# Optimization experiments

Measured on AMD Instinct MI355X. Metric: run time of the kernel, lower is better.

Reference implementation:

```python
import jax, jax.numpy as jnp
import numpy as np
from jax import lax

S = 2048      # services
MAXL = 16     # max exec steps per service
D = 4096      # devices
RN = 128      # size_realnode
HN = 128      # size_hypernode
HEADS = 4
CH = RN + HN  # 256
NRO = 256     # readout neurons
NITER = 3
NEG = 0.2     # leaky relu slope


def _gru(x, h, Wih, Whh, bih, bhh):
    # PyTorch GRU/GRUCell equations, gate order (r, z, n)
    gi = x @ Wih + bih
    gh = h @ Whh + bhh
    ir, iz, ig = jnp.split(gi, 3, axis=-1)
    hr, hz, hg = jnp.split(gh, 3, axis=-1)
    r = jax.nn.sigmoid(ir + hr)
    z = jax.nn.sigmoid(iz + hz)
    n = jnp.tanh(ig + r * hg)
    return (1.0 - z) * n + z * h


def _mlp(x, W1, b1, W2, b2, W3, b3):
    # Linear-ReLU-(Dropout eval=id)-Linear-ReLU-Linear
    h = jax.nn.relu(x @ W1 + b1)
    h = jax.nn.relu(h @ W2 + b2)
    return h @ W3 + b3


def forward(realnode, arr, exeSeqs, index_devices, index_fragments, frag2dev_node, frag2dev_row, lengths, frag_service, frag_pos,
            W_dev, b_dev, W_frg, b_frg, W_srv, b_srv,
            C_Wih, C_Whh, C_bih, C_bhh, F_Wih, F_Whh, F_bih, F_bhh, D_Wih, D_Whh, D_bih, D_bhh,
            W_src, b_src, W_tgt, b_tgt, att, bias_att,
            Wt1, bt1, Wt2, bt2, Wt3, bt3, Wl1, bl1, Wl2, bl2, Wl3, bl3):
    nodes = realnode.shape[0] + 1          # row 0 is zero-pad row (1-based node ids)
    Sn, L2 = exeSeqs.shape
    L = L2 // 2
    Dn = index_devices.shape[0]
    dtype = realnode.dtype

    # initial real-node states (scatter with disjoint indices == set)
    devs = realnode[index_devices - 1] @ W_dev + b_dev
    frags = realnode[index_fragments - 1] @ W_frg + b_frg
    state = jnp.zeros((nodes, RN), dtype).at[index_devices].set(devs).at[index_fragments].set(frags)

    h_srv = arr @ W_srv + b_srv            # [S, HN] GRU hidden (torch shape [1,S,HN])
    frag_state = state[index_fragments]

    for _ in range(NITER):
        # phiC: packed GRU over per-service execution sequences
        seq = state[exeSeqs].reshape(Sn, L, 2 * RN)   # [S, L, 2*RN]

        def step(h, xt_t):
            xt, t = xt_t
            hn = _gru(xt, h, C_Wih, C_Whh, C_bih, C_bhh)
            h = jnp.where((t < lengths)[:, None], hn, h)  # packed semantics: freeze past length
            return h, h

        h_srv, outs = lax.scan(step, h_srv, (seq.transpose(1, 0, 2), jnp.arange(L)))
        outs = outs.transpose(1, 0, 2)                # [S, L, HN]
        out_f = outs[frag_service, frag_pos]          # [F, HN] valid steps only (extract_indices)

        # messageF: hypernode output || state of device hosting the fragment
        msgF = jnp.concatenate([out_f, state[frag2dev_node]], axis=-1)   # [F, HN+RN]
        frag_state = state[index_fragments]
        frag_old = frag_state
        frag_state = _gru(msgF, frag_state, F_Wih, F_Whh, F_bih, F_bhh)

        # GAT-style scatter softmax over devices
        src = (jnp.concatenate([out_f, frag_old], axis=-1) @ W_src + b_src).reshape(-1, HEADS, CH)  # [F,H,CH]
        dev_state = state[index_devices]
        tgt = (dev_state @ W_tgt + b_tgt).reshape(-1, HEADS, CH)                                    # [D,H,CH]
        e = jax.nn.leaky_relu(src + tgt[frag2dev_row], NEG)
        alpha = (e * att).sum(-1)                                        # [F, HEADS]
        amax = jax.ops.segment_max(alpha, frag2dev_row, num_segments=Dn)
        w = jnp.exp(alpha - amax[frag2dev_row])
        wsum = jax.ops.segment_sum(w, frag2dev_row, num_segments=Dn)
        a = w / (wsum[frag2dev_row] + 1e-16)
        msgD = jax.ops.segment_sum(src * a[:, :, None], frag2dev_row, num_segments=Dn)
        msgD = msgD.mean(axis=1) + bias_att                              # [D, CH]
        dev_state = _gru(msgD, dev_state, D_Wih, D_Whh, D_bih, D_bhh)

        state = jnp.zeros((nodes, RN), dtype).at[index_devices].set(dev_state).at[index_fragments].set(frag_state)

    # mean-pool fragment states per service
    pooled = jax.ops.segment_sum(frag_state, frag_service, num_segments=Sn) / lengths[:, None].astype(dtype)
    latency = _mlp(pooled, Wl1, bl1, Wl2, bl2, Wl3, bl3)[:, 0]           # [S]
    thr = _mlp(h_srv, Wt1, bt1, Wt2, bt2, Wt3, bt3)[:, 0]                # [S]
    return jnp.concatenate([latency, thr])[None, :]                      # [1, 2S]


def setup_inputs() -> dict:
    lengths_np = np.tile(np.array([4, 8, 12, 16], dtype=np.int64), S // 4)
    F = int(lengths_np.sum())            # 20480 fragments
    num_real = D + F                     # 24576
    rng = np.random.RandomState(0)
    frag2dev_row = rng.randint(0, D, size=F).astype(np.int64)       # device row per fragment
    frag_service = np.repeat(np.arange(S, dtype=np.int64), lengths_np)
    frag_pos = np.concatenate([np.arange(l, dtype=np.int64) for l in lengths_np])
    index_devices = np.arange(1, D + 1, dtype=np.int64)             # 1-based node ids
    index_fragments = np.arange(D + 1, D + F + 1, dtype=np.int64)
    dev_node = frag2dev_row + 1
    exeSeqs = np.zeros((S, 2 * MAXL), dtype=np.int64)               # pad with 0 (zero row)
    exeSeqs[frag_service, 2 * frag_pos] = index_fragments
    exeSeqs[frag_service, 2 * frag_pos + 1] = dev_node

    keys = iter(jax.random.split(jax.random.key(0), 64))
    def rn(shape, s=0.05):
        return jax.random.normal(next(keys), shape, jnp.float32) * s
    z = lambda *sh: jnp.zeros(sh, jnp.float32)

    return {
        'realnode': rn((num_real, 5), 1.0), 'arr': rn((S, 5), 1.0),
        'exeSeqs': jnp.asarray(exeSeqs), 'index_devices': jnp.asarray(index_devices),
        'index_fragments': jnp.asarray(index_fragments), 'frag2dev_node': jnp.asarray(dev_node),
        'frag2dev_row': jnp.asarray(frag2dev_row), 'lengths': jnp.asarray(lengths_np),
        'frag_service': jnp.asarray(frag_service), 'frag_pos': jnp.asarray(frag_pos),
        'W_dev': rn((5, RN), 0.3), 'b_dev': z(RN), 'W_frg': rn((5, RN), 0.3), 'b_frg': z(RN),
        'W_srv': rn((5, HN), 0.3), 'b_srv': z(HN),
        'C_Wih': rn((2 * RN, 3 * HN)), 'C_Whh': rn((HN, 3 * HN)), 'C_bih': z(3 * HN), 'C_bhh': z(3 * HN),
        'F_Wih': rn((CH, 3 * RN)), 'F_Whh': rn((RN, 3 * RN)), 'F_bih': z(3 * RN), 'F_bhh': z(3 * RN),
        'D_Wih': rn((CH, 3 * RN)), 'D_Whh': rn((RN, 3 * RN)), 'D_bih': z(3 * RN), 'D_bhh': z(3 * RN),
        'W_src': rn((CH, HEADS * CH)), 'b_src': z(HEADS * CH),
        'W_tgt': rn((RN, HEADS * CH)), 'b_tgt': z(HEADS * CH),
        'att': rn((1, HEADS, CH), 0.1), 'bias_att': z(CH),
        'Wt1': rn((HN, NRO)), 'bt1': z(NRO), 'Wt2': rn((NRO, NRO)), 'bt2': z(NRO), 'Wt3': rn((NRO, 1)), 'bt3': z(1),
        'Wl1': rn((RN, NRO)), 'bl1': z(NRO), 'Wl2': rn((NRO, NRO)), 'bl2': z(NRO), 'Wl3': rn((NRO, 1)), 'bl3': z(1),
    }


def reference(realnode, arr, exeSeqs, index_devices, index_fragments, frag2dev_node, frag2dev_row, lengths, frag_service, frag_pos,
              W_dev, b_dev, W_frg, b_frg, W_srv, b_srv,
              C_Wih, C_Whh, C_bih, C_bhh, F_Wih, F_Whh, F_bih, F_bhh, D_Wih, D_Whh, D_bih, D_bhh,
              W_src, b_src, W_tgt, b_tgt, att, bias_att,
              Wt1, bt1, Wt2, bt2, Wt3, bt3, Wl1, bl1, Wl2, bl2, Wl3, bl3):
    return forward(realnode, arr, exeSeqs, index_devices, index_fragments, frag2dev_node, frag2dev_row, lengths, frag_service, frag_pos,
                   W_dev, b_dev, W_frg, b_frg, W_srv, b_srv,
                   C_Wih, C_Whh, C_bih, C_bhh, F_Wih, F_Whh, F_bih, F_bhh, D_Wih, D_Whh, D_bih, D_bhh,
                   W_src, b_src, W_tgt, b_tgt, att, bias_att,
                   Wt1, bt1, Wt2, bt2, Wt3, bt3, Wl1, bl1, Wl2, bl2, Wl3, bl3)
```

## Files before the change

kernel.cpp:

```cpp
#include <hip/hip_runtime.h>
#include <hip/hip_bf16.h>

typedef __attribute__((ext_vector_type(8))) short bf16x8;
typedef __attribute__((ext_vector_type(4))) float f32x4;

__device__ __forceinline__ float sigf(float x){ return 1.0f/(1.0f+expf(-x)); }
__device__ __forceinline__ int clampi(int v, int lo, int hi){ return v<lo?lo:(v>hi?hi:v); }
__device__ __forceinline__ unsigned short f2b(float f){
    __hip_bfloat16 h = __float2bfloat16(f);
    return *reinterpret_cast<unsigned short*>(&h);
}
__device__ __forceinline__ float us2f(unsigned short u){ return __uint_as_float(((unsigned)u)<<16); }

__device__ __forceinline__ void gload16(const void* g, void* l){
    __builtin_amdgcn_global_load_lds((const __attribute__((address_space(1))) void*)g,
                                     (__attribute__((address_space(3))) void*)l, 16, 0, 0);
}

__global__ void k_cvt(const int* __restrict__ src, int* __restrict__ dst, int n,
                      const int* __restrict__ det)
{
    int i = blockIdx.x*blockDim.x + threadIdx.x;
    if (i >= n) return;
    int stride = (det[1] == 0) ? 2 : 1;
    dst[i] = src[(size_t)i*stride];
}

__global__ void k_wt(const float* __restrict__ W, unsigned short* __restrict__ Wt,
                     int N, int kshift, int kmask, int total)
{
    int idx = blockIdx.x*blockDim.x + threadIdx.x;
    if (idx >= total) return;
    int n = idx >> kshift, k = idx & kmask;
    Wt[idx] = f2b(W[(size_t)k*N + n]);
}

__global__ void k_wt2(const float* __restrict__ W, unsigned short* __restrict__ Whi,
                      unsigned short* __restrict__ Wlo, int N, int kshift, int kmask, int total)
{
    int idx = blockIdx.x*blockDim.x + threadIdx.x;
    if (idx >= total) return;
    int n = idx >> kshift, k = idx & kmask;
    float v = W[(size_t)k*N + n];
    unsigned short hi = f2b(v);
    Whi[idx] = hi;
    Wlo[idx] = f2b(v - us2f(hi));
}

__global__ void k_proj5(const float* __restrict__ X, const float* __restrict__ W,
                        const float* __restrict__ bias,
                        const int* __restrict__ gidx, const int* __restrict__ sidx,
                        float* __restrict__ out, unsigned short* __restrict__ outBf,
                        float* __restrict__ out2, unsigned short* __restrict__ out2Bf,
                        int M, int nrows, int nodes)
{
    int t = blockIdx.x*blockDim.x + threadIdx.x;
    int i = t >> 7, j = t & 127;
    if (i >= M) return;
    int src = gidx ? clampi(gidx[i]-1, 0, nrows-1) : i;
    const float* xp = X + (size_t)src*5;
    float acc = bias[j];
#pragma unroll
    for (int k=0;k<5;k++) acc += xp[k] * W[k*128+j];
    int dr = sidx ? clampi(sidx[i], 0, nodes-1) : i;
    if (out)   out[(size_t)dr*128 + j] = acc;
    if (outBf) outBf[(size_t)dr*128 + j] = f2b(acc);
    if (out2)  out2[(size_t)i*128 + j] = acc;
    if (out2Bf) out2Bf[(size_t)i*128 + j] = f2b(acc);
}

__launch_bounds__(256)
__global__ void k_mm(const float* __restrict__ A0, int lda,
                     const float* __restrict__ B, int ldb,
                     const float* __restrict__ bias, float* __restrict__ C,
                     int M, int N, int K, int relu, float scale, int accum)
{
    __shared__ float As[16][132];
    __shared__ float Bs[16][132];
    int tid = threadIdx.x;
    int tx = tid & 15, ty = tid >> 4;
    int row0 = blockIdx.y * 128, col0 = blockIdx.x * 128;
    float acc[8][8] = {};
    for (int k0 = 0; k0 < K; k0 += 16){
#pragma unroll
        for (int q = 0; q < 2; ++q){
            int idx = tid + q*256;
            int r = idx >> 2, k4 = (idx & 3) * 4;
            const float* src = A0 + (size_t)(row0+r)*lda + k0 + k4;
            float4 v = *reinterpret_cast<const float4*>(src);
            As[k4+0][r]=v.x; As[k4+1][r]=v.y; As[k4+2][r]=v.z; As[k4+3][r]=v.w;
        }
#pragma unroll
        for (int q = 0; q < 2; ++q){
            int idx = tid + q*256;
            int kb = idx >> 5, n4 = (idx & 31) * 4;
            float4 v = *reinterpret_cast<const float4*>(B + (size_t)(k0+kb)*ldb + col0 + n4);
            *reinterpret_cast<float4*>(&Bs[kb][n4]) = v;
        }
        __syncthreads();
#pragma unroll
        for (int k = 0; k < 16; ++k){
            float a[8], b[8];
            *(float4*)&a[0] = *(const float4*)&As[k][ty*8];
            *(float4*)&a[4] = *(const float4*)&As[k][ty*8+4];
            *(float4*)&b[0] = *(const float4*)&Bs[k][tx*8];
            *(float4*)&b[4] = *(const float4*)&Bs[k][tx*8+4];
#pragma unroll
            for (int i=0;i<8;i++)
#pragma unroll
                for (int j=0;j<8;j++) acc[i][j] += a[i]*b[j];
        }
        __syncthreads();
    }
    float bb[8];
#pragma unroll
    for (int j=0;j<8;j++) bb[j] = bias ? bias[col0+tx*8+j] : 0.f;
#pragma unroll
    for (int i=0;i<8;i++){
        float* cp = C + (size_t)(row0+ty*8+i)*N + col0 + tx*8;
#pragma unroll
        for (int jq=0;jq<2;jq++){
            float4 prev = accum ? *(const float4*)(cp+jq*4) : make_float4(0,0,0,0);
            float o[4];
#pragma unroll
            for (int c=0;c<4;c++){
                float u = acc[i][jq*4+c] + bb[jq*4+c];
                if (relu) u = fmaxf(u,0.f);
                o[c] = (&prev.x)[c] + scale*u;
            }
            *(float4*)(cp+jq*4) = make_float4(o[0],o[1],o[2],o[3]);
        }
    }
}

struct MJob {
    const unsigned short *A0, *A1;
    const int *i0, *i1;
    const unsigned short *Wt;
    const float *bias;
    void *C;
    int N, K, epi, nrow;
    float scale;
};

#define MM2_SMEM 67840

__device__ __forceinline__ void mm2_body(const MJob J, int bid, char* smem)
{
    unsigned short* AsB = (unsigned short*)smem;
    unsigned short* BsB = AsB + 16384;
    int tid = threadIdx.x;
    int l = tid & 63, w = tid >> 6;
    int wr = w >> 1, wc = w & 1;
    int row0 = (bid % J.nrow) * 128, col0 = (bid / J.nrow) * 128;
    int nK = J.K >> 6;

    f32x4 acc[4][4];
#pragma unroll
    for (int m=0;m<4;m++)
#pragma unroll
        for (int n=0;n<4;n++) acc[m][n] = (f32x4){0.f,0.f,0.f,0.f};

    auto stage = [&](int buf, int k0){
        unsigned short* As = AsB + buf*8192;
        unsigned short* Bs = BsB + buf*8192;
#pragma unroll
        for (int q=0;q<4;q++){
            int slot = q*256 + w*64 + l;
            int r = slot >> 3, c8 = slot & 7;
            int g8 = c8 ^ (r & 7);
            int row; const unsigned short* base; int kl;
            if (k0 < 128){ row = J.i0 ? J.i0[row0+r] : (row0+r); base = J.A0; kl = k0; }
            else         { row = J.i1 ? J.i1[row0+r] : (row0+r); base = J.A1; kl = k0-128; }
            const char* g = (const char*)(base + (size_t)row*128 + kl) + g8*16;
            gload16(g, (void*)&As[(size_t)(q*256 + w*64)*8]);
        }
#pragma unroll
        for (int q=0;q<4;q++){
            int slot = q*256 + w*64 + l;
            int n = slot >> 3, kc = slot & 7;
            int g8 = kc ^ (n & 7);
            const char* g = (const char*)(J.Wt + (size_t)(col0+n)*J.K + k0) + g8*16;
            gload16(g, (void*)&Bs[(size_t)(q*256 + w*64)*8]);
        }
    };

    stage(0, 0);
    for (int ks=0; ks<nK; ++ks){
        int cur = ks & 1;
        if (ks+1 < nK){
            stage(cur^1, (ks+1)*64);
            asm volatile("s_waitcnt vmcnt(8)" ::: "memory");
        } else {
            asm volatile("s_waitcnt vmcnt(0)" ::: "memory");
        }
        __builtin_amdgcn_s_barrier();
        __builtin_amdgcn_sched_barrier(0);
        unsigned short* As = AsB + cur*8192;
        unsigned short* Bs = BsB + cur*8192;
#pragma unroll
        for (int kk = 0; kk < 2; ++kk){
            int ek = kk*32 + (l >> 4) * 8;
            bf16x8 af[4], bf[4];
#pragma unroll
            for (int m=0;m<4;m++){
                int r = wr*64 + m*16 + (l & 15);
                af[m] = *reinterpret_cast<const bf16x8*>(&As[r*64 + (ek ^ ((r & 7) << 3))]);
            }
#pragma unroll
            for (int n=0;n<4;n++){
                int c = wc*64 + n*16 + (l & 15);
                bf[n] = *reinterpret_cast<const bf16x8*>(&Bs[c*64 + (ek ^ ((c & 7) << 3))]);
            }
#pragma unroll
            for (int m=0;m<4;m++)
#pragma unroll
                for (int n=0;n<4;n++)
                    acc[m][n] = __builtin_amdgcn_mfma_f32_16x16x32_bf16(af[m], bf[n], acc[m][n], 0, 0, 0);
        }
        __builtin_amdgcn_sched_barrier(0);
        __builtin_amdgcn_s_barrier();
    }

    if (J.epi == 0){
        float* Ct = (float*)smem;
#pragma unroll
        for (int m=0;m<4;m++){
#pragma unroll
            for (int v=0;v<4;v++){
                int rl = wr*64 + m*16 + (l >> 4)*4 + v;
#pragma unroll
                for (int n=0;n<4;n++){
                    int c = wc*64 + n*16 + (l & 15);
                    Ct[rl*132 + c] = J.scale*acc[m][n][v] + (J.bias ? J.bias[col0+c] : 0.f);
                }
            }
        }
        __syncthreads();
#pragma unroll
        for (int q=0;q<16;q++){
            int idx = tid + q*256;
            int r = idx >> 5, c4 = (idx & 31)*4;
            float4 v = *reinterpret_cast<const float4*>(&Ct[r*132 + c4]);
            *reinterpret_cast<float4*>((float*)J.C + (size_t)(row0+r)*J.N + col0 + c4) = v;
        }
    } else {
        unsigned short* Cb = (unsigned short*)smem;
#pragma unroll
        for (int m=0;m<4;m++){
#pragma unroll
            for (int v=0;v<4;v++){
                int rl = wr*64 + m*16 + (l >> 4)*4 + v;
#pragma unroll
                for (int n=0;n<4;n++){
                    int c = wc*64 + n*16 + (l & 15);
                    Cb[rl*136 + c] = f2b(J.scale*acc[m][n][v] + (J.bias ? J.bias[col0+c] : 0.f));
                }
            }
        }
        __syncthreads();
#pragma unroll
        for (int q=0;q<8;q++){
            int idx = tid + q*256;
            int r = idx >> 4, c8 = (idx & 15)*8;
            uint4 v = *reinterpret_cast<const uint4*>(&Cb[r*136 + c8]);
            *reinterpret_cast<uint4*>((unsigned short*)J.C + (size_t)(row0+r)*J.N + col0 + c8) = v;
        }
    }
}

__launch_bounds__(256)
__global__ void mm2one(MJob a)
{
    __shared__ alignas(16) char smem[MM2_SMEM];
    mm2_body(a, blockIdx.x, smem);
}

__launch_bounds__(256)
__global__ void mm2two(MJob a, MJob b, int asplit)
{
    __shared__ alignas(16) char smem[MM2_SMEM];
    int bid = blockIdx.x;
    if (bid < asplit) mm2_body(a, bid, smem);
    else              mm2_body(b, bid - asplit, smem);
}

struct GJob {
    const unsigned short *A0, *A1;
    const int *i0, *i1;
    int lda;
    const unsigned short *Wih, *Whh;
    const float *bih, *bhh;
    float *H;
    unsigned short *Hbf, *stateBf;
    const int *sidx;
    int M, nodes;
};

__device__ __forceinline__ void gru_body(const GJob J, int bid, char* smem)
{
    unsigned short* AsB = (unsigned short*)smem;
    unsigned short* BsB = AsB + 2*8192;
    int tid = threadIdx.x;
    int l = tid & 63, w = tid >> 6;
    int row0 = bid * 128;
    f32x4 acc[24], accN[8];
#pragma unroll
    for (int n=0;n<24;n++) acc[n] = (f32x4){0.f,0.f,0.f,0.f};
#pragma unroll
    for (int n=0;n<8;n++) accN[n] = (f32x4){0.f,0.f,0.f,0.f};

    auto stage = [&](int buf, int st){
        int k0 = st*64;
        unsigned short* As = AsB + buf*8192;
        unsigned short* Bs = BsB + buf*24576;
#pragma unroll
        for (int q=0;q<2;q++){
            int slot = q*512 + w*64 + l;
            int r = slot >> 3, c8 = slot & 7;
            int g8 = c8 ^ (r & 7);
            const unsigned short* src;
            if (st < 4){
                if (J.i1){
                    if (k0 < 128){ int ri = J.i0 ? J.i0[row0+r] : (row0+r); src = J.A0 + (size_t)ri*128 + k0; }
                    else         { int ri = J.i1[row0+r]; src = J.A1 + (size_t)ri*128 + (k0-128); }
                } else {
                    src = J.A0 + (size_t)(row0+r)*J.lda + k0;
                }
            } else {
                src = J.Hbf + (size_t)(row0+r)*128 + (k0-256);
            }
            gload16((const char*)src + g8*16, (void*)&As[(size_t)(q*512 + w*64)*8]);
        }
#pragma unroll
        for (int q=0;q<6;q++){
            int slot = q*512 + w*64 + l;
            int n = slot >> 3, kc = slot & 7;
            int g8 = kc ^ (n & 7);
            const unsigned short* src = (st < 4) ? (J.Wih + (size_t)n*256 + k0)
                                                 : (J.Whh + (size_t)n*128 + (k0-256));
            gload16((const char*)src + g8*16, (void*)&Bs[(size_t)(q*512 + w*64)*8]);
        }
    };

    stage(0, 0);
    for (int st=0; st<6; ++st){
        int cur = st & 1;
        if (st+1 < 6){
            stage(cur^1, st+1);
            asm volatile("s_waitcnt vmcnt(8)" ::: "memory");
        } else {
            asm volatile("s_waitcnt vmcnt(0)" ::: "memory");
        }
        __builtin_amdgcn_s_barrier();
        __builtin_amdgcn_sched_barrier(0);
        unsigned short* As = AsB + cur*8192;
        unsigned short* Bs = BsB + cur*24576;
        if (st < 4){
#pragma unroll
            for (int kk=0; kk<2; ++kk){
                int ek = kk*32 + (l >> 4)*8;
                int r = w*16 + (l & 15);
                bf16x8 af = *reinterpret_cast<const bf16x8*>(&As[r*64 + (ek ^ ((r & 7) << 3))]);
#pragma unroll
                for (int n=0;n<24;n++){
                    int c = n*16 + (l & 15);
                    bf16x8 bf = *reinterpret_cast<const bf16x8*>(&Bs[c*64 + (ek ^ ((c & 7) << 3))]);
                    acc[n] = __builtin_amdgcn_mfma_f32_16x16x32_bf16(af, bf, acc[n], 0, 0, 0);
                }
            }
        } else {
#pragma unroll
            for (int kk=0; kk<2; ++kk){
                int ek = kk*32 + (l >> 4)*8;
                int r = w*16 + (l & 15);
                bf16x8 af = *reinterpret_cast<const bf16x8*>(&As[r*64 + (ek ^ ((r & 7) << 3))]);
#pragma unroll
                for (int n=0;n<24;n++){
                    int c = n*16 + (l & 15);
                    bf16x8 bf = *reinterpret_cast<const bf16x8*>(&Bs[c*64 + (ek ^ ((c & 7) << 3))]);
                    if (n < 16) acc[n]     = __builtin_amdgcn_mfma_f32_16x16x32_bf16(af, bf, acc[n], 0, 0, 0);
                    else        accN[n-16] = __builtin_amdgcn_mfma_f32_16x16x32_bf16(af, bf, accN[n-16], 0, 0, 0);
                }
            }
        }
        __builtin_amdgcn_sched_barrier(0);
        __builtin_amdgcn_s_barrier();
    }

    __syncthreads();
    float* Hld = (float*)smem;
    unsigned short* Hb = (unsigned short*)(smem + 67584);
#pragma unroll
    for (int q=0;q<8;q++){
        int idx = tid + q*512;
        int r = idx >> 5, c4 = (idx & 31)*4;
        float4 v = *reinterpret_cast<const float4*>(J.H + (size_t)(row0+r)*128 + c4);
        *reinterpret_cast<float4*>(&Hld[r*132 + c4]) = v;
    }
    __syncthreads();
#pragma unroll
    for (int v=0;v<4;v++){
        int rl = w*16 + (l >> 4)*4 + v;
#pragma unroll
        for (int c=0;c<8;c++){
            int col = c*16 + (l & 15);
            float rr = sigf(acc[c][v]    + J.bih[col]     + J.bhh[col]);
            float zz = sigf(acc[c+8][v]  + J.bih[col+128] + J.bhh[col+128]);
            float nn = tanhf(acc[c+16][v] + J.bih[col+256] + rr*(accN[c][v] + J.bhh[col+256]));
            float hv = Hld[rl*132 + col];
            float hn = (1.f-zz)*nn + zz*hv;
            Hld[rl*132 + col] = hn;
            Hb[rl*136 + col] = f2b(hn);
        }
    }
    __syncthreads();
#pragma unroll
    for (int q=0;q<8;q++){
        int idx = tid + q*512;
        int r = idx >> 5, c4 = (idx & 31)*4;
        float4 v = *reinterpret_cast<const float4*>(&Hld[r*132 + c4]);
        *reinterpret_cast<float4*>(J.H + (size_t)(row0+r)*128 + c4) = v;
    }
#pragma unroll
    for (int q=0;q<4;q++){
        int idx = tid + q*512;
        int r = idx >> 4, c8 = (idx & 15)*8;
        uint4 v = *reinterpret_cast<const uint4*>(&Hb[r*136 + c8]);
        *reinterpret_cast<uint4*>(J.Hbf + (size_t)(row0+r)*128 + c8) = v;
        int st = clampi(J.sidx[row0+r],0,J.nodes-1);
        *reinterpret_cast<uint4*>(J.stateBf + (size_t)st*128 + c8) = v;
    }
}

__launch_bounds__(512)
__global__ void gru2(GJob a, GJob b, int asplit)
{
    __shared__ alignas(16) char smem[131072];
    int bid = blockIdx.x;
    if (bid < asplit) gru_body(a, bid, smem);
    else              gru_body(b, bid - asplit, smem);
}

__launch_bounds__(256)
__global__ void k_attn(const unsigned short* __restrict__ SRC, const unsigned short* __restrict__ tgtbf,
                       const float* __restrict__ att, const int* __restrict__ list,
                       const int* __restrict__ offs, const float* __restrict__ batt,
                       unsigned short* __restrict__ msgDbf,
                       float* __restrict__ alphaG, int Dn, int F)
{
    __shared__ float tg[1024];
    __shared__ float alds[128*4];
    __shared__ float accs[4][256];
    int d = blockIdx.x;
    int tid = threadIdx.x;
    int w = tid >> 6, lane = tid & 63;
    for (int u = tid; u < 1024; u += 256) tg[u] = us2f(tgtbf[(size_t)d*1024 + u]);
    __syncthreads();
    int beg = offs[d], end = offs[d+1];
    if (beg < 0) beg = 0; if (end > F) end = F; if (end < beg) end = beg;
    int c0 = w*256 + lane*4;
    float t0 = tg[c0], t1 = tg[c0+1], t2 = tg[c0+2], t3 = tg[c0+3];
    float a0 = att[c0], a1 = att[c0+1], a2 = att[c0+2], a3 = att[c0+3];
    float amax = -3.4e38f;
    for (int i=beg;i<end;i++){
        int f = list[i];
        ushort4 sv = *reinterpret_cast<const ushort4*>(SRC + (size_t)f*1024 + c0);
        float e0 = us2f(sv.x)+t0, e1 = us2f(sv.y)+t1, e2 = us2f(sv.z)+t2, e3 = us2f(sv.w)+t3;
        e0 = e0>0.f?e0:0.2f*e0; e1 = e1>0.f?e1:0.2f*e1;
        e2 = e2>0.f?e2:0.2f*e2; e3 = e3>0.f?e3:0.2f*e3;
        float s = e0*a0 + e1*a1 + e2*a2 + e3*a3;
#pragma unroll
        for (int msk=1; msk<64; msk<<=1) s += __shfl_xor(s, msk);
        int li = i - beg;
        if (li < 128){ if (lane == 0) alds[li*4+w] = s; }
        else         { if (lane == 0) alphaG[(size_t)f*4+w] = s; }
        amax = fmaxf(amax, s);
    }
    __syncthreads();
    float wsum = 0.f;
    for (int i=beg;i<end;i++){
        int li = i - beg;
        float a = (li < 128) ? alds[li*4+w] : alphaG[(size_t)list[i]*4+w];
        wsum += expf(a - amax);
    }
    float iws = 1.f/(wsum + 1e-16f);
    float acc[4] = {0,0,0,0};
    for (int i=beg;i<end;i++){
        int f = list[i];
        int li = i - beg;
        float a = (li < 128) ? alds[li*4+w] : alphaG[(size_t)f*4+w];
        float p = expf(a - amax)*iws;
        ushort4 sv = *reinterpret_cast<const ushort4*>(SRC + (size_t)f*1024 + c0);
        acc[0] += p*us2f(sv.x); acc[1] += p*us2f(sv.y);
        acc[2] += p*us2f(sv.z); acc[3] += p*us2f(sv.w);
    }
#pragma unroll
    for (int j=0;j<4;j++) accs[w][lane*4+j] = acc[j];
    __syncthreads();
    if (tid < 256){
        float m = (accs[0][tid]+accs[1][tid]+accs[2][tid]+accs[3][tid])*0.25f + batt[tid];
        msgDbf[(size_t)d*256 + tid] = f2b(m);
    }
}

__launch_bounds__(512)
__global__ void k_recur(float* __restrict__ h_srv, const unsigned short* __restrict__ giFb,
                        const unsigned short* __restrict__ Whi,
                        const unsigned short* __restrict__ Wlo,
                        const float* __restrict__ bhh,
                        const int* __restrict__ inv,
                        unsigned short* __restrict__ out_f_bf,
                        int S, int L, int F)
{
    __shared__ float hs[8][129];
    __shared__ alignas(16) unsigned short hsHi[16*128];
    __shared__ alignas(16) unsigned short hsLo[16*128];
    __shared__ float ghs[16][385];
    __shared__ int fLoc[16][8];
    int tid = threadIdx.x;
    int l = tid & 63, w = tid >> 6;
    int lane15 = l & 15, lhi = l >> 4;
    int s0 = blockIdx.x * 8;
    for (int u = tid; u < 2048; u += 512){
        int s=u>>7,k=u&127;
        int ksw = k ^ ((s & 7) << 3);
        if (s < 8){
            float v = h_srv[(size_t)(s0+s)*128+k];
            hs[s][k] = v;
            unsigned short hb = f2b(v);
            hsHi[s*128 + ksw] = hb;
            hsLo[s*128 + ksw] = f2b(v - us2f(hb));
        } else {
            hsHi[s*128 + ksw] = 0;
            hsLo[s*128 + ksw] = 0;
        }
    }
    if (tid < 128) fLoc[tid>>3][tid&7] = inv[(size_t)(s0+(tid&7))*L + (tid>>3)];
    bf16x8 wHi[3][4], wLo[3][4];
#pragma unroll
    for (int ct=0; ct<3; ++ct){
        int col = w*48 + ct*16 + lane15;
#pragma unroll
        for (int ks=0; ks<4; ++ks){
            size_t off = (size_t)col*128 + ks*32 + lhi*8;
            wHi[ct][ks] = *reinterpret_cast<const bf16x8*>(Whi + off);
            wLo[ct][ks] = *reinterpret_cast<const bf16x8*>(Wlo + off);
        }
    }
    __syncthreads();
    for (int t=0;t<L;++t){
        bf16x8 hHi[4], hLo[4];
#pragma unroll
        for (int ks=0; ks<4; ++ks){
            int ek = ks*32 + lhi*8;
            int off = lane15*128 + (ek ^ ((lane15 & 7) << 3));
            hHi[ks] = *reinterpret_cast<const bf16x8*>(&hsHi[off]);
            hLo[ks] = *reinterpret_cast<const bf16x8*>(&hsLo[off]);
        }
#pragma unroll
        for (int ct=0; ct<3; ++ct){
            f32x4 acc = (f32x4){0.f,0.f,0.f,0.f};
#pragma unroll
            for (int ks=0; ks<4; ++ks){
                acc = __builtin_amdgcn_mfma_f32_16x16x32_bf16(hHi[ks], wHi[ct][ks], acc, 0,0,0);
                acc = __builtin_amdgcn_mfma_f32_16x16x32_bf16(hLo[ks], wHi[ct][ks], acc, 0,0,0);
                acc = __builtin_amdgcn_mfma_f32_16x16x32_bf16(hHi[ks], wLo[ct][ks], acc, 0,0,0);
            }
            int col = w*48 + ct*16 + lane15;
            float bb = bhh[col];
#pragma unroll
            for (int v=0; v<4; ++v){
                ghs[lhi*4 + v][col] = acc[v] + bb;
            }
        }
        __syncthreads();
        for (int u = tid; u < 1024; u += 512){
            int s=u>>7, k=u&127; int f = fLoc[t][s];
            if (f >= 0 && f < F){
                const unsigned short* gp = giFb + (size_t)f*384;
                float r  = sigf(us2f(gp[k])     + ghs[s][k]);
                float zz = sigf(us2f(gp[128+k]) + ghs[s][128+k]);
                float n  = tanhf(us2f(gp[256+k]) + r*ghs[s][256+k]);
                float hn = (1.f-zz)*n + zz*hs[s][k];
                hs[s][k] = hn;
                unsigned short hb = f2b(hn);
                int ksw = k ^ ((s & 7) << 3);
                hsHi[s*128 + ksw] = hb;
                hsLo[s*128 + ksw] = f2b(hn - us2f(hb));
                out_f_bf[(size_t)f*128+k] = hb;
            }
        }
        __syncthreads();
    }
    for (int u = tid; u < 1024; u += 512){ int s=u>>7,k=u&127; h_srv[(size_t)(s0+s)*128+k] = hs[s][k]; }
}

__global__ void k_count(const int* __restrict__ row, int* __restrict__ counts, int F, int Dn)
{ int f = blockIdx.x*blockDim.x + threadIdx.x; if (f < F) atomicAdd(&counts[clampi(row[f],0,Dn-1)], 1); }

__global__ void k_scan(const int* __restrict__ counts, int* __restrict__ offs, int D)
{
    __shared__ int part[257];
    int tid = threadIdx.x;
    int per = (D + 255) / 256;
    int s = 0;
    for (int i=0;i<per;i++){ int idx = tid*per+i; if (idx < D) s += counts[idx]; }
    part[tid] = s;
    __syncthreads();
    if (tid == 0){
        int acc = 0;
        for (int i=0;i<256;i++){ int v = part[i]; part[i] = acc; acc += v; }
        part[256] = acc;
    }
    __syncthreads();
    int acc = part[tid];
    for (int i=0;i<per;i++){ int idx = tid*per+i; if (idx < D){ offs[idx] = acc; acc += counts[idx]; } }
    if (tid == 0) offs[D] = part[256];
}

__global__ void k_fill(const int* __restrict__ row, const int* __restrict__ offs,
                       int* __restrict__ cursor, int* __restrict__ list, int F, int Dn)
{
    int f = blockIdx.x*blockDim.x + threadIdx.x;
    if (f >= F) return;
    int r = clampi(row[f],0,Dn-1);
    int p = atomicAdd(&cursor[r], 1);
    int pos = offs[r]+p;
    if (pos >= 0 && pos < F) list[pos] = f;
}

__global__ void k_build_inv(const int* __restrict__ fs, const int* __restrict__ fp,
                            int* __restrict__ inv, int F, int L, int S)
{
    int f = blockIdx.x*blockDim.x + threadIdx.x;
    if (f >= F) return;
    inv[clampi(fs[f],0,S-1)*L + clampi(fp[f],0,L-1)] = f;
}

__global__ void k_pool_add(const float* __restrict__ frag, const int* __restrict__ fs,
                           float* __restrict__ pooled, int F, int S)
{
    int t = blockIdx.x*blockDim.x + threadIdx.x;
    int i = t >> 7, j = t & 127;
    if (i >= F) return;
    atomicAdd(&pooled[(size_t)clampi(fs[i],0,S-1)*128 + j], frag[(size_t)i*128 + j]);
}

__global__ void k_pool_div(float* __restrict__ pooled, const int* __restrict__ lengths, int S)
{
    int t = blockIdx.x*blockDim.x + threadIdx.x;
    int i = t >> 7, j = t & 127;
    if (i >= S) return;
    int l = lengths[i]; if (l < 1) l = 1;
    pooled[(size_t)i*128 + j] /= (float)l;
}

__global__ void k_dot_out(const float* __restrict__ H, const float* __restrict__ W3,
                          const float* __restrict__ b3, float* __restrict__ outv, int off)
{
    __shared__ float red[256];
    int s = blockIdx.x, tid = threadIdx.x;
    red[tid] = H[(size_t)s*256 + tid] * W3[tid];
    __syncthreads();
    for (int st=128; st; st>>=1){ if (tid < st) red[tid] += red[tid+st]; __syncthreads(); }
    if (tid == 0) outv[off + s] = red[0] + b3[0];
}

extern "C" void kernel_launch(void* const* d_in, const int* in_sizes, int n_in,
                              void* d_out, int out_size, void* d_ws, size_t ws_size,
                              hipStream_t stream)
{
    (void)n_in; (void)out_size; (void)ws_size;
    const float* realnode = (const float*)d_in[0];
    const float* arr      = (const float*)d_in[1];
    const int* r_exe   = (const int*)d_in[2];
    const int* r_idev  = (const int*)d_in[3];
    const int* r_ifrag = (const int*)d_in[4];
    const int* r_fdn   = (const int*)d_in[5];
    const int* r_fdr   = (const int*)d_in[6];
    const int* r_len   = (const int*)d_in[7];
    const int* r_fsvc  = (const int*)d_in[8];
    const int* r_fpos  = (const int*)d_in[9];
    const float *W_dev=(const float*)d_in[10], *b_dev=(const float*)d_in[11];
    const float *W_frg=(const float*)d_in[12], *b_frg=(const float*)d_in[13];
    const float *W_srv=(const float*)d_in[14], *b_srv=(const float*)d_in[15];
    const float *C_Wih=(const float*)d_in[16], *C_Whh=(const float*)d_in[17], *C_bih=(const float*)d_in[18], *C_bhh=(const float*)d_in[19];
    const float *F_Wih=(const float*)d_in[20], *F_Whh=(const float*)d_in[21], *F_bih=(const float*)d_in[22], *F_bhh=(const float*)d_in[23];
    const float *D_Wih=(const float*)d_in[24], *D_Whh=(const float*)d_in[25], *D_bih=(const float*)d_in[26], *D_bhh=(const float*)d_in[27];
    const float *W_src=(const float*)d_in[28], *b_src=(const float*)d_in[29];
    const float *W_tgt=(const float*)d_in[30], *b_tgt=(const float*)d_in[31];
    const float *att=(const float*)d_in[32], *bias_att=(const float*)d_in[33];
    const float *Wt1=(const float*)d_in[34], *bt1=(const float*)d_in[35], *Wt2=(const float*)d_in[36], *bt2=(const float*)d_in[37], *Wt3=(const float*)d_in[38], *bt3=(const float*)d_in[39];
    const float *Wl1=(const float*)d_in[40], *bl1=(const float*)d_in[41], *Wl2=(const float*)d_in[42], *bl2=(const float*)d_in[43], *Wl3=(const float*)d_in[44], *bl3=(const float*)d_in[45];
    float* outp = (float*)d_out;

    const int S  = in_sizes[7];
    const int Dn = in_sizes[3];
    const int F  = in_sizes[4];
    const int L  = in_sizes[2] / (2*S);
    const int nreal = in_sizes[0]/5;
    const int nodes = nreal + 1;
    const int NIT = 3;

    char* wp = (char*)d_ws;
    auto alloc = [&](size_t nelem)->float*{
        float* p = (float*)wp;
        wp += ((nelem*4 + 255)/256)*256;
        return p;
    };
    float* h_srv  = alloc((size_t)S*128);
    float* fragA  = alloc((size_t)F*128);
    float* devA   = alloc((size_t)Dn*128);
    float* alphaB = alloc((size_t)F*4);
    float* UNION  = alloc((size_t)F*512);
    unsigned short* giFb = (unsigned short*)UNION;
    unsigned short* SRC  = (unsigned short*)UNION;
    float* Z      = alloc((size_t)Dn*1024);
    float* TGTf   = alloc((size_t)Dn*512);
    unsigned short* TGT = (unsigned short*)TGTf;
    float* pooled = alloc((size_t)S*128);
    unsigned short* state_bf = (unsigned short*)alloc((size_t)nodes*64);
    unsigned short* out_f_bf = (unsigned short*)alloc((size_t)F*64);
    unsigned short* fragA_bf = (unsigned short*)alloc((size_t)F*64);
    unsigned short* devA_bf  = (unsigned short*)alloc((size_t)Dn*64);
    unsigned short* msgD_bf  = (unsigned short*)alloc((size_t)Dn*128);
    unsigned short* tCWih   = (unsigned short*)alloc(384*256/2);
    unsigned short* tCWhhHi = (unsigned short*)alloc(384*128/2);
    unsigned short* tCWhhLo = (unsigned short*)alloc(384*128/2);
    unsigned short* tFWih   = (unsigned short*)alloc(384*256/2);
    unsigned short* tFWhh   = (unsigned short*)alloc(384*128/2);
    unsigned short* tDWih   = (unsigned short*)alloc(384*256/2);
    unsigned short* tDWhh   = (unsigned short*)alloc(384*128/2);
    unsigned short* tWtgt   = (unsigned short*)alloc(1024*128/2);
    unsigned short* tWsrc   = (unsigned short*)alloc(1024*256/2);
    int* cExe   = (int*)alloc((size_t)S*2*L);
    int* cIdev  = (int*)alloc((size_t)Dn);
    int* cIfrag = (int*)alloc((size_t)F);
    int* cFdn   = (int*)alloc((size_t)F);
    int* cFdr   = (int*)alloc((size_t)F);
    int* cLen   = (int*)alloc((size_t)S);
    int* cFsvc  = (int*)alloc((size_t)F);
    int* cFpos  = (int*)alloc((size_t)F);
    int* inv    = (int*)alloc((size_t)S*L);
    int* counts = (int*)alloc((size_t)Dn);
    int* offs   = (int*)alloc((size_t)Dn+1);
    int* cursor = (int*)alloc((size_t)Dn);
    int* list   = (int*)alloc((size_t)F);

    const int* det = r_idev;
    auto cvt = [&](const int* src, int* dst, int n){
        k_cvt<<<dim3((n+255)/256),256,0,stream>>>(src, dst, n, det);
    };
    cvt(r_exe,  cExe,  S*2*L);
    cvt(r_idev, cIdev, Dn);
    cvt(r_ifrag,cIfrag,F);
    cvt(r_fdn,  cFdn,  F);
    cvt(r_fdr,  cFdr,  F);
    cvt(r_len,  cLen,  S);
    cvt(r_fsvc, cFsvc, F);
    cvt(r_fpos, cFpos, F);

    k_wt<<<dim3((98304+255)/256),256,0,stream>>>(C_Wih, tCWih, 384, 8, 255, 98304);
    k_wt2<<<dim3((49152+255)/256),256,0,stream>>>(C_Whh, tCWhhHi, tCWhhLo, 384, 7, 127, 49152);
    k_wt<<<dim3((98304+255)/256),256,0,stream>>>(F_Wih, tFWih, 384, 8, 255, 98304);
    k_wt<<<dim3((49152+255)/256),256,0,stream>>>(F_Whh, tFWhh, 384, 7, 127, 49152);
    k_wt<<<dim3((98304+255)/256),256,0,stream>>>(D_Wih, tDWih, 384, 8, 255, 98304);
    k_wt<<<dim3((49152+255)/256),256,0,stream>>>(D_Whh, tDWhh, 384, 7, 127, 49152);
    k_wt<<<dim3((131072+255)/256),256,0,stream>>>(W_tgt, tWtgt, 1024, 7, 127, 131072);
    k_wt<<<dim3((262144+255)/256),256,0,stream>>>(W_src, tWsrc, 1024, 8, 255, 262144);

    hipMemsetAsync(state_bf, 0, (size_t)nodes*128*2, stream);
    hipMemsetAsync(inv, 0xFF, (size_t)S*L*4, stream);
    hipMemsetAsync(counts, 0, (size_t)Dn*4, stream);
    hipMemsetAsync(cursor, 0, (size_t)Dn*4, stream);

    k_proj5<<<dim3((Dn*128+255)/256),256,0,stream>>>(realnode, W_dev, b_dev, cIdev, cIdev,
        nullptr, state_bf, devA, devA_bf, Dn, nreal, nodes);
    k_proj5<<<dim3(((size_t)F*128+255)/256),256,0,stream>>>(realnode, W_frg, b_frg, cIfrag, cIfrag,
        nullptr, state_bf, fragA, fragA_bf, F, nreal, nodes);
    k_proj5<<<dim3((S*128+255)/256),256,0,stream>>>(arr, W_srv, b_srv, nullptr, nullptr,
        h_srv, nullptr, nullptr, nullptr, S, S, nodes);
    k_build_inv<<<dim3((F+255)/256),256,0,stream>>>(cFsvc, cFpos, inv, F, L, S);
    k_count<<<dim3((F+255)/256),256,0,stream>>>(cFdr, counts, F, Dn);
    k_scan<<<1,256,0,stream>>>(counts, offs, Dn);
    k_fill<<<dim3((F+255)/256),256,0,stream>>>(cFdr, offs, cursor, list, F, Dn);

    const int nrF = F/128, nrD = Dn/128;
    MJob jGi  = { state_bf, state_bf, cIfrag, cFdn, tCWih, C_bih, giFb, 384, 256, 2, nrF, 1.f };
    MJob jTgt = { devA_bf, devA_bf, nullptr, nullptr, tWtgt, b_tgt, TGT, 1024, 128, 2, nrD, 1.f };
    MJob jSrc = { out_f_bf, fragA_bf, nullptr, nullptr, tWsrc, b_src, SRC, 1024, 256, 2, nrF, 1.f };
    GJob jF = { out_f_bf, state_bf, nullptr, cFdn, 128, tFWih, tFWhh, F_bih, F_bhh,
                fragA, fragA_bf, state_bf, cIfrag, F, nodes };
    GJob jD = { msgD_bf, nullptr, nullptr, nullptr, 256, tDWih, tDWhh, D_bih, D_bhh,
                devA, devA_bf, state_bf, cIdev, Dn, nodes };

    for (int it=0; it<NIT; ++it){
        mm2two<<<dim3(3*nrF + 8*nrD),256,0,stream>>>(jGi, jTgt, 3*nrF);
        k_recur<<<dim3(S/8),512,0,stream>>>(h_srv, giFb, tCWhhHi, tCWhhLo, C_bhh, inv,
            out_f_bf, S, L, F);
        mm2one<<<dim3(8*nrF),256,0,stream>>>(jSrc);
        k_attn<<<dim3(Dn),256,0,stream>>>(SRC, TGT, att, list, offs, bias_att,
            msgD_bf, alphaB, Dn, F);
        gru2<<<dim3(nrF + nrD),512,0,stream>>>(jF, jD, nrF);
    }

    hipMemsetAsync(pooled, 0, (size_t)S*128*4, stream);
    k_pool_add<<<dim3(((size_t)F*128+255)/256),256,0,stream>>>(fragA, cFsvc, pooled, F, S);
    k_pool_div<<<dim3((S*128+255)/256),256,0,stream>>>(pooled, cLen, S);
    float* h1 = (float*)TGTf;
    k_mm<<<dim3(256/128, S/128),256,0,stream>>>(pooled, 128, Wl1, 256, bl1, h1, S, 256, 128, 1, 1.f, 0);
    k_mm<<<dim3(256/128, S/128),256,0,stream>>>(h1, 256, Wl2, 256, bl2, Z, S, 256, 256, 1, 1.f, 0);
    k_dot_out<<<dim3(S),256,0,stream>>>(Z, Wl3, bl3, outp, 0);
    k_mm<<<dim3(256/128, S/128),256,0,stream>>>(h_srv, 128, Wt1, 256, bt1, h1, S, 256, 128, 1, 1.f, 0);
    k_mm<<<dim3(256/128, S/128),256,0,stream>>>(h1, 256, Wt2, 256, bt2, Z, S, 256, 256, 1, 1.f, 0);
    k_dot_out<<<dim3(S),256,0,stream>>>(Z, Wt3, bt3, outp, S);
}
```

Before: 800.9 us.

## Halve GRU kernel LDS by using K=32 stages and a two-pass epilogue

The GRU GEMM pipeline now stages 32-wide K slices instead of 64 across 12 stages, with 4-way XOR swizzle, which halves the double-buffered LDS tiles. The epilogue processes the 128-row hidden-state tile in two 64-row halves so its LDS scratch also fits. Shared memory drops from 128KB to 64KB, which lets two blocks share a CU on hardware with 160KB of LDS. In exchange there are more barriers per tile and shorter prefetch distance, and half the warps sit idle during each epilogue pass.

```diff
diff --git a/kernel.cpp b/kernel.cpp
--- a/kernel.cpp
+++ b/kernel.cpp
@@ -300,7 +300,7 @@
 __device__ __forceinline__ void gru_body(const GJob J, int bid, char* smem)
 {
     unsigned short* AsB = (unsigned short*)smem;
-    unsigned short* BsB = AsB + 2*8192;
+    unsigned short* BsB = AsB + 8192;
     int tid = threadIdx.x;
     int l = tid & 63, w = tid >> 6;
     int row0 = bid * 128;
@@ -311,16 +311,14 @@
     for (int n=0;n<8;n++) accN[n] = (f32x4){0.f,0.f,0.f,0.f};
 
     auto stage = [&](int buf, int st){
-        int k0 = st*64;
-        unsigned short* As = AsB + buf*8192;
-        unsigned short* Bs = BsB + buf*24576;
-#pragma unroll
-        for (int q=0;q<2;q++){
-            int slot = q*512 + w*64 + l;
-            int r = slot >> 3, c8 = slot & 7;
-            int g8 = c8 ^ (r & 7);
+        int k0 = st*32;
+        unsigned short* As = AsB + buf*4096;
+        unsigned short* Bs = BsB + buf*12288;
+        {
+            int r = tid >> 2, c4 = tid & 3;
+            int g4 = c4 ^ (r & 3);
             const unsigned short* src;
-            if (st < 4){
+            if (st < 8){
                 if (J.i1){
                     if (k0 < 128){ int ri = J.i0 ? J.i0[row0+r] : (row0+r); src = J.A0 + (size_t)ri*128 + k0; }
                     else         { int ri = J.i1[row0+r]; src = J.A1 + (size_t)ri*128 + (k0-128); }
@@ -330,58 +328,49 @@
             } else {
                 src = J.Hbf + (size_t)(row0+r)*128 + (k0-256);
             }
-            gload16((const char*)src + g8*16, (void*)&As[(size_t)(q*512 + w*64)*8]);
-        }
-#pragma unroll
-        for (int q=0;q<6;q++){
-            int slot = q*512 + w*64 + l;
-            int n = slot >> 3, kc = slot & 7;
-            int g8 = kc ^ (n & 7);
-            const unsigned short* src = (st < 4) ? (J.Wih + (size_t)n*256 + k0)
+            gload16((const char*)src + g4*16, (void*)&As[(size_t)(w*64)*8]);
+        }
+#pragma unroll
+        for (int q=0;q<3;q++){
+            int slot = q*512 + tid;
+            int n = slot >> 2, c4 = slot & 3;
+            int g4 = c4 ^ (n & 3);
+            const unsigned short* src = (st < 8) ? (J.Wih + (size_t)n*256 + k0)
                                                  : (J.Whh + (size_t)n*128 + (k0-256));
-            gload16((const char*)src + g8*16, (void*)&Bs[(size_t)(q*512 + w*64)*8]);
+            gload16((const char*)src + g4*16, (void*)&Bs[(size_t)(q*512 + w*64)*8]);
         }
     };
 
     stage(0, 0);
-    for (int st=0; st<6; ++st){
+    for (int st=0; st<12; ++st){
         int cur = st & 1;
-        if (st+1 < 6){
+        if (st+1 < 12){
             stage(cur^1, st+1);
-            asm volatile("s_waitcnt vmcnt(8)" ::: "memory");
+            asm volatile("s_waitcnt vmcnt(4)" ::: "memory");
         } else {
             asm volatile("s_waitcnt vmcnt(0)" ::: "memory");
         }
         __builtin_amdgcn_s_barrier();
         __builtin_amdgcn_sched_barrier(0);
-        unsigned short* As = AsB + cur*8192;
-        unsigned short* Bs = BsB + cur*24576;
-        if (st < 4){
-#pragma unroll
-            for (int kk=0; kk<2; ++kk){
-                int ek = kk*32 + (l >> 4)*8;
-                int r = w*16 + (l & 15);
-                bf16x8 af = *reinterpret_cast<const bf16x8*>(&As[r*64 + (ek ^ ((r & 7) << 3))]);
-#pragma unroll
-                for (int n=0;n<24;n++){
-                    int c = n*16 + (l & 15);
-                    bf16x8 bf = *reinterpret_cast<const bf16x8*>(&Bs[c*64 + (ek ^ ((c & 7) << 3))]);
-                    acc[n] = __builtin_amdgcn_mfma_f32_16x16x32_bf16(af, bf, acc[n], 0, 0, 0);
-                }
+        unsigned short* As = AsB + cur*4096;
+        unsigned short* Bs = BsB + cur*12288;
+        int ek = (l >> 4) * 8;
+        int r = w*16 + (l & 15);
+        bf16x8 af = *reinterpret_cast<const bf16x8*>(&As[r*32 + (ek ^ ((r & 3) << 3))]);
+        if (st < 8){
+#pragma unroll
+            for (int n=0;n<24;n++){
+                int c = n*16 + (l & 15);
+                bf16x8 bf = *reinterpret_cast<const bf16x8*>(&Bs[c*32 + (ek ^ ((c & 3) << 3))]);
+                acc[n] = __builtin_amdgcn_mfma_f32_16x16x32_bf16(af, bf, acc[n], 0, 0, 0);
             }
         } else {
 #pragma unroll
-            for (int kk=0; kk<2; ++kk){
-                int ek = kk*32 + (l >> 4)*8;
-                int r = w*16 + (l & 15);
-                bf16x8 af = *reinterpret_cast<const bf16x8*>(&As[r*64 + (ek ^ ((r & 7) << 3))]);
-#pragma unroll
-                for (int n=0;n<24;n++){
-                    int c = n*16 + (l & 15);
-                    bf16x8 bf = *reinterpret_cast<const bf16x8*>(&Bs[c*64 + (ek ^ ((c & 7) << 3))]);
-                    if (n < 16) acc[n]     = __builtin_amdgcn_mfma_f32_16x16x32_bf16(af, bf, acc[n], 0, 0, 0);
-                    else        accN[n-16] = __builtin_amdgcn_mfma_f32_16x16x32_bf16(af, bf, accN[n-16], 0, 0, 0);
-                }
+            for (int n=0;n<24;n++){
+                int c = n*16 + (l & 15);
+                bf16x8 bf = *reinterpret_cast<const bf16x8*>(&Bs[c*32 + (ek ^ ((c & 3) << 3))]);
+                if (n < 16) acc[n]     = __builtin_amdgcn_mfma_f32_16x16x32_bf16(af, bf, acc[n], 0, 0, 0);
+                else        accN[n-16] = __builtin_amdgcn_mfma_f32_16x16x32_bf16(af, bf, accN[n-16], 0, 0, 0);
             }
         }
         __builtin_amdgcn_sched_barrier(0);
@@ -390,53 +379,60 @@
 
     __syncthreads();
     float* Hld = (float*)smem;
-    unsigned short* Hb = (unsigned short*)(smem + 67584);
-#pragma unroll
-    for (int q=0;q<8;q++){
-        int idx = tid + q*512;
-        int r = idx >> 5, c4 = (idx & 31)*4;
-        float4 v = *reinterpret_cast<const float4*>(J.H + (size_t)(row0+r)*128 + c4);
-        *reinterpret_cast<float4*>(&Hld[r*132 + c4]) = v;
-    }
-    __syncthreads();
-#pragma unroll
-    for (int v=0;v<4;v++){
-        int rl = w*16 + (l >> 4)*4 + v;
-#pragma unroll
-        for (int c=0;c<8;c++){
-            int col = c*16 + (l & 15);
-            float rr = sigf(acc[c][v]    + J.bih[col]     + J.bhh[col]);
-            float zz = sigf(acc[c+8][v]  + J.bih[col+128] + J.bhh[col+128]);
-            float nn = tanhf(acc[c+16][v] + J.bih[col+256] + rr*(accN[c][v] + J.bhh[col+256]));
-            float hv = Hld[rl*132 + col];
-            float hn = (1.f-zz)*nn + zz*hv;
-            Hld[rl*132 + col] = hn;
-            Hb[rl*136 + col] = f2b(hn);
-        }
-    }
-    __syncthreads();
-#pragma unroll
-    for (int q=0;q<8;q++){
-        int idx = tid + q*512;
-        int r = idx >> 5, c4 = (idx & 31)*4;
-        float4 v = *reinterpret_cast<const float4*>(&Hld[r*132 + c4]);
-        *reinterpret_cast<float4*>(J.H + (size_t)(row0+r)*128 + c4) = v;
-    }
-#pragma unroll
-    for (int q=0;q<4;q++){
-        int idx = tid + q*512;
-        int r = idx >> 4, c8 = (idx & 15)*8;
-        uint4 v = *reinterpret_cast<const uint4*>(&Hb[r*136 + c8]);
-        *reinterpret_cast<uint4*>(J.Hbf + (size_t)(row0+r)*128 + c8) = v;
-        int st = clampi(J.sidx[row0+r],0,J.nodes-1);
-        *reinterpret_cast<uint4*>(J.stateBf + (size_t)st*128 + c8) = v;
+    unsigned short* Hb = (unsigned short*)(smem + 33792);
+#pragma unroll
+    for (int half=0; half<2; ++half){
+        int rbase = half*64;
+#pragma unroll
+        for (int q=0;q<4;q++){
+            int idx = tid + q*512;
+            int r = idx >> 5, c4 = (idx & 31)*4;
+            float4 v = *reinterpret_cast<const float4*>(J.H + (size_t)(row0+rbase+r)*128 + c4);
+            *reinterpret_cast<float4*>(&Hld[r*132 + c4]) = v;
+        }
+        __syncthreads();
+        if ((w >> 2) == half){
+#pragma unroll
+            for (int v=0;v<4;v++){
+                int rloc = (w & 3)*16 + (l >> 4)*4 + v;
+#pragma unroll
+                for (int c=0;c<8;c++){
+                    int col = c*16 + (l & 15);
+                    float rr = sigf(acc[c][v]    + J.bih[col]     + J.bhh[col]);
+                    float zz = sigf(acc[c+8][v]  + J.bih[col+128] + J.bhh[col+128]);
+                    float nn = tanhf(acc[c+16][v] + J.bih[col+256] + rr*(accN[c][v] + J.bhh[col+256]));
+                    float hv = Hld[rloc*132 + col];
+                    float hn = (1.f-zz)*nn + zz*hv;
+                    Hld[rloc*132 + col] = hn;
+                    Hb[rloc*136 + col] = f2b(hn);
+                }
+            }
+        }
+        __syncthreads();
+#pragma unroll
+        for (int q=0;q<4;q++){
+            int idx = tid + q*512;
+            int r = idx >> 5, c4 = (idx & 31)*4;
+            float4 v = *reinterpret_cast<const float4*>(&Hld[r*132 + c4]);
+            *reinterpret_cast<float4*>(J.H + (size_t)(row0+rbase+r)*128 + c4) = v;
+        }
+#pragma unroll
+        for (int q=0;q<2;q++){
+            int idx = tid + q*512;
+            int r = idx >> 4, c8 = (idx & 15)*8;
+            uint4 v = *reinterpret_cast<const uint4*>(&Hb[r*136 + c8]);
+            *reinterpret_cast<uint4*>(J.Hbf + (size_t)(row0+rbase+r)*128 + c8) = v;
+            int st = clampi(J.sidx[row0+rbase+r],0,J.nodes-1);
+            *reinterpret_cast<uint4*>(J.stateBf + (size_t)st*128 + c8) = v;
+        }
+        __syncthreads();
     }
 }
 
 __launch_bounds__(512)
 __global__ void gru2(GJob a, GJob b, int asplit)
 {
-    __shared__ alignas(16) char smem[131072];
+    __shared__ alignas(16) char smem[65536];
     int bid = blockIdx.x;
     if (bid < asplit) gru_body(a, bid, smem);
     else              gru_body(b, bid - asplit, smem);
```

Measured after the change: 921.1 us. 15.0% more time.

## Store GRU tiles in MFMA fragment order and drop fp32 hidden-state copies

Applied to the files above, without the earlier changes.

The GRU kernel now loads A and B tiles into LDS already arranged in MFMA fragment order, replacing the XOR-swizzled layout. Each fragment read becomes a linear per-lane address, which removes the index arithmetic. The fp32 fragment and device hidden-state buffers are removed; the previous hidden state is read from the bf16 copy, and pooling uses the bf16 values. This cuts global traffic and LDS staging in the epilogue, but the recurrent hidden state is now stored only in bf16, which reduces precision across iterations.

```diff
diff --git a/kernel.cpp b/kernel.cpp
--- a/kernel.cpp
+++ b/kernel.cpp
@@ -291,7 +291,6 @@
     int lda;
     const unsigned short *Wih, *Whh;
     const float *bih, *bhh;
-    float *H;
     unsigned short *Hbf, *stateBf;
     const int *sidx;
     int M, nodes;
@@ -316,9 +315,11 @@
         unsigned short* Bs = BsB + buf*24576;
 #pragma unroll
         for (int q=0;q<2;q++){
-            int slot = q*512 + w*64 + l;
-            int r = slot >> 3, c8 = slot & 7;
-            int g8 = c8 ^ (r & 7);
+            int i = q*512 + tid;
+            int frag = i >> 6, lane = i & 63;
+            int kk = frag >> 3, wv = frag & 7;
+            int r = wv*16 + (lane & 15);
+            int slot = kk*4 + ((lane >> 4) & 3);
             const unsigned short* src;
             if (st < 4){
                 if (J.i1){
@@ -330,16 +331,18 @@
             } else {
                 src = J.Hbf + (size_t)(row0+r)*128 + (k0-256);
             }
-            gload16((const char*)src + g8*16, (void*)&As[(size_t)(q*512 + w*64)*8]);
+            gload16((const char*)(src + slot*8), (void*)&As[(size_t)(q*512 + w*64)*8]);
         }
 #pragma unroll
         for (int q=0;q<6;q++){
-            int slot = q*512 + w*64 + l;
-            int n = slot >> 3, kc = slot & 7;
-            int g8 = kc ^ (n & 7);
-            const unsigned short* src = (st < 4) ? (J.Wih + (size_t)n*256 + k0)
-                                                 : (J.Whh + (size_t)n*128 + (k0-256));
-            gload16((const char*)src + g8*16, (void*)&Bs[(size_t)(q*512 + w*64)*8]);
+            int i = q*512 + tid;
+            int frag = i >> 6, lane = i & 63;
+            int kk = frag / 24, n = frag % 24;
+            int col = n*16 + (lane & 15);
+            int slot = kk*4 + ((lane >> 4) & 3);
+            const unsigned short* src = (st < 4) ? (J.Wih + (size_t)col*256 + k0)
+                                                 : (J.Whh + (size_t)col*128 + (k0-256));
+            gload16((const char*)(src + slot*8), (void*)&Bs[(size_t)(q*512 + w*64)*8]);
         }
     };
 
@@ -359,26 +362,20 @@
         if (st < 4){
 #pragma unroll
             for (int kk=0; kk<2; ++kk){
-                int ek = kk*32 + (l >> 4)*8;
-                int r = w*16 + (l & 15);
-                bf16x8 af = *reinterpret_cast<const bf16x8*>(&As[r*64 + (ek ^ ((r & 7) << 3))]);
+                bf16x8 af = *reinterpret_cast<const bf16x8*>(&As[(size_t)((kk*8 + w)*64 + l)*8]);
 #pragma unroll
                 for (int n=0;n<24;n++){
-                    int c = n*16 + (l & 15);
-                    bf16x8 bf = *reinterpret_cast<const bf16x8*>(&Bs[c*64 + (ek ^ ((c & 7) << 3))]);
+                    bf16x8 bf = *reinterpret_cast<const bf16x8*>(&Bs[(size_t)((kk*24 + n)*64 + l)*8]);
                     acc[n] = __builtin_amdgcn_mfma_f32_16x16x32_bf16(af, bf, acc[n], 0, 0, 0);
                 }
             }
         } else {
 #pragma unroll
             for (int kk=0; kk<2; ++kk){
-                int ek = kk*32 + (l >> 4)*8;
-                int r = w*16 + (l & 15);
-                bf16x8 af = *reinterpret_cast<const bf16x8*>(&As[r*64 + (ek ^ ((r & 7) << 3))]);
+                bf16x8 af = *reinterpret_cast<const bf16x8*>(&As[(size_t)((kk*8 + w)*64 + l)*8]);
 #pragma unroll
                 for (int n=0;n<24;n++){
-                    int c = n*16 + (l & 15);
-                    bf16x8 bf = *reinterpret_cast<const bf16x8*>(&Bs[c*64 + (ek ^ ((c & 7) << 3))]);
+                    bf16x8 bf = *reinterpret_cast<const bf16x8*>(&Bs[(size_t)((kk*24 + n)*64 + l)*8]);
                     if (n < 16) acc[n]     = __builtin_amdgcn_mfma_f32_16x16x32_bf16(af, bf, acc[n], 0, 0, 0);
                     else        accN[n-16] = __builtin_amdgcn_mfma_f32_16x16x32_bf16(af, bf, accN[n-16], 0, 0, 0);
                 }
@@ -389,39 +386,30 @@
     }
 
     __syncthreads();
-    float* Hld = (float*)smem;
-    unsigned short* Hb = (unsigned short*)(smem + 67584);
-#pragma unroll
-    for (int q=0;q<8;q++){
+    unsigned short* Hb = (unsigned short*)smem;
+#pragma unroll
+    for (int q=0;q<4;q++){
         int idx = tid + q*512;
-        int r = idx >> 5, c4 = (idx & 31)*4;
-        float4 v = *reinterpret_cast<const float4*>(J.H + (size_t)(row0+r)*128 + c4);
-        *reinterpret_cast<float4*>(&Hld[r*132 + c4]) = v;
+        int r = idx >> 4, c8 = (idx & 15)*8;
+        uint4 v = *reinterpret_cast<const uint4*>(J.Hbf + (size_t)(row0+r)*128 + c8);
+        *reinterpret_cast<uint4*>(&Hb[r*136 + c8]) = v;
     }
     __syncthreads();
 #pragma unroll
     for (int v=0;v<4;v++){
-        int rl = w*16 + (l >> 4)*4 + v;
+        int rloc = w*16 + (l >> 4)*4 + v;
 #pragma unroll
         for (int c=0;c<8;c++){
             int col = c*16 + (l & 15);
             float rr = sigf(acc[c][v]    + J.bih[col]     + J.bhh[col]);
             float zz = sigf(acc[c+8][v]  + J.bih[col+128] + J.bhh[col+128]);
             float nn = tanhf(acc[c+16][v] + J.bih[col+256] + rr*(accN[c][v] + J.bhh[col+256]));
-            float hv = Hld[rl*132 + col];
+            float hv = us2f(Hb[rloc*136 + col]);
             float hn = (1.f-zz)*nn + zz*hv;
-            Hld[rl*132 + col] = hn;
-            Hb[rl*136 + col] = f2b(hn);
-        }
-    }
-    __syncthreads();
-#pragma unroll
-    for (int q=0;q<8;q++){
-        int idx = tid + q*512;
-        int r = idx >> 5, c4 = (idx & 31)*4;
-        float4 v = *reinterpret_cast<const float4*>(&Hld[r*132 + c4]);
-        *reinterpret_cast<float4*>(J.H + (size_t)(row0+r)*128 + c4) = v;
-    }
+            Hb[rloc*136 + col] = f2b(hn);
+        }
+    }
+    __syncthreads();
 #pragma unroll
     for (int q=0;q<4;q++){
         int idx = tid + q*512;
@@ -638,13 +626,13 @@
     inv[clampi(fs[f],0,S-1)*L + clampi(fp[f],0,L-1)] = f;
 }
 
-__global__ void k_pool_add(const float* __restrict__ frag, const int* __restrict__ fs,
+__global__ void k_pool_add(const unsigned short* __restrict__ fragBf, const int* __restrict__ fs,
                            float* __restrict__ pooled, int F, int S)
 {
     int t = blockIdx.x*blockDim.x + threadIdx.x;
     int i = t >> 7, j = t & 127;
     if (i >= F) return;
-    atomicAdd(&pooled[(size_t)clampi(fs[i],0,S-1)*128 + j], frag[(size_t)i*128 + j]);
+    atomicAdd(&pooled[(size_t)clampi(fs[i],0,S-1)*128 + j], us2f(fragBf[(size_t)i*128 + j]));
 }
 
 __global__ void k_pool_div(float* __restrict__ pooled, const int* __restrict__ lengths, int S)
@@ -710,8 +698,6 @@
         return p;
     };
     float* h_srv  = alloc((size_t)S*128);
-    float* fragA  = alloc((size_t)F*128);
-    float* devA   = alloc((size_t)Dn*128);
     float* alphaB = alloc((size_t)F*4);
     float* UNION  = alloc((size_t)F*512);
     unsigned short* giFb = (unsigned short*)UNION;
@@ -776,9 +762,9 @@
     hipMemsetAsync(cursor, 0, (size_t)Dn*4, stream);
 
     k_proj5<<<dim3((Dn*128+255)/256),256,0,stream>>>(realnode, W_dev, b_dev, cIdev, cIdev,
-        nullptr, state_bf, devA, devA_bf, Dn, nreal, nodes);
+        nullptr, state_bf, nullptr, devA_bf, Dn, nreal, nodes);
     k_proj5<<<dim3(((size_t)F*128+255)/256),256,0,stream>>>(realnode, W_frg, b_frg, cIfrag, cIfrag,
-        nullptr, state_bf, fragA, fragA_bf, F, nreal, nodes);
+        nullptr, state_bf, nullptr, fragA_bf, F, nreal, nodes);
     k_proj5<<<dim3((S*128+255)/256),256,0,stream>>>(arr, W_srv, b_srv, nullptr, nullptr,
         h_srv, nullptr, nullptr, nullptr, S, S, nodes);
     k_build_inv<<<dim3((F+255)/256),256,0,stream>>>(cFsvc, cFpos, inv, F, L, S);
@@ -791,9 +777,9 @@
     MJob jTgt = { devA_bf, devA_bf, nullptr, nullptr, tWtgt, b_tgt, TGT, 1024, 128, 2, nrD, 1.f };
     MJob jSrc = { out_f_bf, fragA_bf, nullptr, nullptr, tWsrc, b_src, SRC, 1024, 256, 2, nrF, 1.f };
     GJob jF = { out_f_bf, state_bf, nullptr, cFdn, 128, tFWih, tFWhh, F_bih, F_bhh,
-                fragA, fragA_bf, state_bf, cIfrag, F, nodes };
+                fragA_bf, state_bf, cIfrag, F, nodes };
     GJob jD = { msgD_bf, nullptr, nullptr, nullptr, 256, tDWih, tDWhh, D_bih, D_bhh,
-                devA, devA_bf, state_bf, cIdev, Dn, nodes };
+                devA_bf, state_bf, cIdev, Dn, nodes };
 
     for (int it=0; it<NIT; ++it){
         mm2two<<<dim3(3*nrF + 8*nrD),256,0,stream>>>(jGi, jTgt, 3*nrF);
@@ -806,7 +792,7 @@
     }
 
     hipMemsetAsync(pooled, 0, (size_t)S*128*4, stream);
-    k_pool_add<<<dim3(((size_t)F*128+255)/256),256,0,stream>>>(fragA, cFsvc, pooled, F, S);
+    k_pool_add<<<dim3(((size_t)F*128+255)/256),256,0,stream>>>(fragA_bf, cFsvc, pooled, F, S);
     k_pool_div<<<dim3((S*128+255)/256),256,0,stream>>>(pooled, cLen, S);
     float* h1 = (float*)TGTf;
     k_mm<<<dim3(256/128, S/128),256,0,stream>>>(pooled, 128, Wl1, 256, bl1, h1, S, 256, 128, 1, 1.f, 0);
```

After: 805.0 us. Within noise of the previous version (+0.5%).
